# Optimization experiments

Hardware: AMD Instinct MI355X
Metric: run time of the kernel (lower is better)

The kernel has to match this reference:

```python
import jax, jax.numpy as jnp
import numpy as np

EPS = 1e-5

def mean_variance_norm(x):
    # x: [b,c,h,w]; torch .var(dim=2) on flattened spatial is UNBIASED (n-1)
    b, c, h, w = x.shape
    n = h * w
    mean = jnp.mean(x, axis=(2, 3), keepdims=True)
    var = jnp.sum((x - mean) ** 2, axis=(2, 3), keepdims=True) / (n - 1) + EPS
    return (x - mean) / jnp.sqrt(var)

def conv1x1(x, W, b):
    # 1x1 conv == channel-mixing matmul. W: [out_c, in_c], b: [out_c]
    return jnp.einsum('oc,bchw->bohw', W, x) + b[None, :, None, None]

def setup_inputs() -> dict:
    key = jax.random.key(0)
    ks = jax.random.split(key, 10)
    C = 512
    shp = (4, C, 64, 64)
    std = 1.0 / np.sqrt(C)
    return {
        'content': jax.random.normal(ks[0], shp, jnp.float32),
        'style': jax.random.normal(ks[1], shp, jnp.float32),
        'Wf': jax.random.normal(ks[2], (C, C), jnp.float32) * std,
        'bf': jax.random.normal(ks[3], (C,), jnp.float32) * 0.01,
        'Wg': jax.random.normal(ks[4], (C, C), jnp.float32) * std,
        'bg': jax.random.normal(ks[5], (C,), jnp.float32) * 0.01,
        'Wh': jax.random.normal(ks[6], (C, C), jnp.float32) * std,
        'bh': jax.random.normal(ks[7], (C,), jnp.float32) * 0.01,
        'Wo': jax.random.normal(ks[8], (C, C), jnp.float32) * std,
        'bo': jax.random.normal(ks[9], (C,), jnp.float32) * 0.01,
    }

def reference(content, style, Wf, bf, Wg, bg, Wh, bh, Wo, bo):
    b, c, h, w = content.shape
    hw = h * w
    F = conv1x1(mean_variance_norm(content), Wf, bf).reshape(b, c, hw)  # queries
    G = conv1x1(mean_variance_norm(style), Wg, bg).reshape(b, c, hw)    # keys
    H = conv1x1(style, Wh, bh).reshape(b, c, hw)                        # values
    # S[b,n,m] = sum_c F[b,c,n] * G[b,c,m]  (unscaled attention scores)
    S = jnp.einsum('bcn,bcm->bnm', F, G)
    S = jax.nn.softmax(S, axis=-1)
    # O[b,c,n] = sum_m H[b,c,m] * S[b,n,m]
    O = jnp.einsum('bcm,bnm->bcn', H, S).reshape(b, c, h, w)
    O = conv1x1(O, Wo, bo)
    return O + content
```

## Files before the change

### kernel.cpp

```cpp
#include <hip/hip_runtime.h>

#define C 512
#define HW 4096
#define EPSV 1e-5f

typedef _Float16 fp16x8 __attribute__((ext_vector_type(8)));
typedef _Float16 fp16x4 __attribute__((ext_vector_type(4)));
typedef float f32x4 __attribute__((ext_vector_type(4)));

#define OFF_MC    (0)
#define OFF_RC    (8192)
#define OFF_MS    (16384)
#define OFF_RS    (24576)
#define OFF_BETAF (32768)
#define OFF_V     (40960)
#define OFF_BZ    (49152)
#define OFF_T     (65536)
#define OFF_SP    (131072)
#define OFF_A     (OFF_SP + 2097152)
#define OFF_WZ    (OFF_A + 1048576)
#define OFF_XCT   (OFF_WZ + 1048576)
#define OFF_XST   (OFF_XCT + 16777216)
#define OFF_KT    (OFF_XST + 16777216)
#define OFF_HM    (OFF_KT + 16777216)
#define OFF_ML    (OFF_HM + 16777216)
#define OFF_S     (OFF_ML + 8388608)

#define FT_IDX(n, c) ((((size_t)((n) >> 4) * 16 + ((c) >> 5)) * 512) + \
                      ((((c) >> 3) & 3) * 128) + (((n) & 15) * 8) + ((c) & 7))

#define SFT_IDX(n, m) ((((size_t)((n) >> 4) * 128 + ((m) >> 5)) * 512) + \
                       ((((m) >> 3) & 3) * 128) + (((n) & 15) * 8) + ((m) & 7))


__global__ void transpose_stats_kernel(const float* __restrict__ xc, const float* __restrict__ xs,
                                       char* __restrict__ ws)
{
    int bx = blockIdx.x;
    int tensor = bx >> 11, b = (bx >> 9) & 3, c0 = ((bx >> 6) & 7) * 64, n0 = (bx & 63) * 64;
    const float* src = tensor ? xs : xc;
    _Float16* dst = (_Float16*)(ws + (tensor ? OFF_XST : OFF_XCT));
    float2* part = (float2*)(ws + OFF_SP);

    __shared__ _Float16 tile[64][72];
    __shared__ float sred[4][64], ssred[4][64];

    int tid = threadIdx.x, cR = tid & 63, ng = tid >> 6;
    const float* p = src + ((size_t)(b * C + c0 + cR)) * HW + n0 + ng * 16;
    float s = 0.f, ss = 0.f;
    #pragma unroll
    for (int k = 0; k < 4; k++) {
        float4 v = *(const float4*)(p + k * 4);
        s += v.x + v.y + v.z + v.w;
        ss += v.x * v.x + v.y * v.y + v.z * v.z + v.w * v.w;
        int n = ng * 16 + k * 4;
        tile[n][cR] = (_Float16)v.x; tile[n + 1][cR] = (_Float16)v.y;
        tile[n + 2][cR] = (_Float16)v.z; tile[n + 3][cR] = (_Float16)v.w;
    }
    sred[ng][cR] = s; ssred[ng][cR] = ss;
    __syncthreads();
    if (tid < 64) {
        float S = sred[0][tid] + sred[1][tid] + sred[2][tid] + sred[3][tid];
        float SS = ssred[0][tid] + ssred[1][tid] + ssred[2][tid] + ssred[3][tid];
        part[((size_t)((tensor * 4 + b) * 512 + c0 + tid)) * 64 + (n0 >> 6)] = make_float2(S, SS);
    }
    _Float16* dstB = dst + (size_t)b * HW * C;
    #pragma unroll
    for (int i = 0; i < 2; i++) {
        int g = tid + i * 256, row = g >> 3, c8 = (g & 7) * 8;
        int n = n0 + row, c = c0 + c8;
        *(fp16x8*)&dstB[FT_IDX(n, c)] = *(const fp16x8*)&tile[row][c8];
    }
}

__global__ void finalize_stats_kernel(char* __restrict__ ws)
{
    int ch = blockIdx.x * 256 + threadIdx.x;
    const float2* part = (const float2*)(ws + OFF_SP) + (size_t)ch * 64;
    float S = 0.f, SS = 0.f;
    for (int k = 0; k < 64; k++) { float2 v = part[k]; S += v.x; SS += v.y; }
    int tensor = ch >> 11, rem = ch & 2047;
    float m = S / (float)HW;
    float var = (SS - S * m) / (float)(HW - 1) + EPSV;
    ((float*)(ws + (tensor ? OFF_MS : OFF_MC)))[rem] = m;
    ((float*)(ws + (tensor ? OFF_RS : OFF_RC)))[rem] = rsqrtf(var);
}

__global__ void precompute_kernel(const float* __restrict__ Wf, const float* __restrict__ Wg,
                                  const float* __restrict__ Wo, const float* __restrict__ Wh,
                                  const float* __restrict__ bf, const float* __restrict__ bh,
                                  char* __restrict__ ws)
{
    float* A = (float*)(ws + OFF_A);
    float* Wz = (float*)(ws + OFF_WZ);
    float* betaf = (float*)(ws + OFF_BETAF);
    float* bz = (float*)(ws + OFF_BZ);
    const float* mc = (const float*)(ws + OFF_MC);
    const float* rc = (const float*)(ws + OFF_RC);
    int bx = blockIdx.x, t = threadIdx.x;
    if (bx < 512) {
        bool isA = bx < 256;
        int r0 = (isA ? bx : bx - 256) * 2;
        float a00 = 0.f, a01 = 0.f, a10 = 0.f, a11 = 0.f;
        for (int k = 0; k < C; k++) {
            float r0v, r1v, c0v, c1v;
            if (isA) {
                r0v = Wf[k * C + r0]; r1v = Wf[k * C + r0 + 1];
                c0v = Wg[k * C + t];  c1v = Wg[k * C + t + 256];
            } else {
                r0v = Wo[r0 * C + k]; r1v = Wo[(r0 + 1) * C + k];
                c0v = Wh[k * C + t];  c1v = Wh[k * C + t + 256];
            }
            a00 += r0v * c0v; a01 += r0v * c1v;
            a10 += r1v * c0v; a11 += r1v * c1v;
        }
        float* D = isA ? A : Wz;
        D[r0 * C + t] = a00;       D[r0 * C + t + 256] = a01;
        D[(r0 + 1) * C + t] = a10; D[(r0 + 1) * C + t + 256] = a11;
    } else if (bx < 520) {
        int g = (bx - 512) * 256 + t, b = g >> 9, co = g & 511;
        float acc = 0.f;
        for (int i = 0; i < C; i++) acc += Wf[co * C + i] * mc[b * C + i] * rc[b * C + i];
        betaf[g] = bf[co] - acc;
    } else {
        int co = (bx - 520) * 256 + t;
        float acc = 0.f;
        for (int i = 0; i < C; i++) acc += Wo[co * C + i] * bh[i];
        bz[co] = acc;
    }
}

__global__ void precompute_v_kernel(const float* __restrict__ Wg, char* __restrict__ ws)
{
    const float* betaf = (const float*)(ws + OFF_BETAF);
    const float* rs = (const float*)(ws + OFF_RS);
    float* v = (float*)(ws + OFF_V);
    int g = blockIdx.x * 32 + (threadIdx.x >> 3);
    int b = g >> 9, j = g & 511, cq = threadIdx.x & 7;
    float acc = 0.f;
    for (int co = cq * 64; co < cq * 64 + 64; co++) acc += betaf[b * C + co] * Wg[co * C + j];
    acc += __shfl_xor(acc, 1);
    acc += __shfl_xor(acc, 2);
    acc += __shfl_xor(acc, 4);
    if (cq == 0) v[g] = rs[b * C + j] * acc;
}

__global__ void __launch_bounds__(256) prep_gemm_kernel(char* __restrict__ ws)
{
    const float* A = (const float*)(ws + OFF_A);
    const float* Wz = (const float*)(ws + OFF_WZ);
    const float* rc = (const float*)(ws + OFF_RC);
    const float* rs = (const float*)(ws + OFF_RS);
    const float* bz = (const float*)(ws + OFF_BZ);
    const _Float16* __restrict__ xsT = (const _Float16*)(ws + OFF_XST);
    _Float16* __restrict__ Kt = (_Float16*)(ws + OFF_KT);
    _Float16* __restrict__ Hp = (_Float16*)(ws + OFF_HM);

    int bx = blockIdx.x;
    int b = bx & 3, rest = bx >> 2;
    int r128 = rest >> 5, mb = rest & 31;
    int r0 = r128 * 128, m0 = mb * 128;
    int w = threadIdx.x >> 6, lane = threadIdx.x & 63, q = lane >> 4, l16 = lane & 15;
    int wr = (w & 1) * 64, wm = (w >> 1) * 64;
    bool isK = (r0 < 512);
    const float* Asrc = isK ? A : Wz;
    int rbase = (isK ? r0 : r0 - 512) + wr;

    f32x4 zz = {0.f, 0.f, 0.f, 0.f};
    f32x4 acc[4][4];
    #pragma unroll
    for (int rt = 0; rt < 4; rt++)
        #pragma unroll
        for (int mt = 0; mt < 4; mt++) acc[rt][mt] = zz;

    float rcv[4];
    #pragma unroll
    for (int rt = 0; rt < 4; rt++)
        rcv[rt] = isK ? rc[b * C + rbase + rt * 16 + l16] : 1.f;

    const _Float16* xb = xsT + (size_t)b * HW * C
                             + (size_t)((m0 + wm) >> 4) * 8192 + q * 128 + l16 * 8;

    for (int ks = 0; ks < 16; ks++) {
        int j0 = ks * 32 + q * 8;
        float rsv[8];
        if (isK) {
            float4 u0 = *(const float4*)&rs[b * C + j0];
            float4 u1 = *(const float4*)&rs[b * C + j0 + 4];
            rsv[0] = u0.x; rsv[1] = u0.y; rsv[2] = u0.z; rsv[3] = u0.w;
            rsv[4] = u1.x; rsv[5] = u1.y; rsv[6] = u1.z; rsv[7] = u1.w;
        } else {
            #pragma unroll
            for (int jj = 0; jj < 8; jj++) rsv[jj] = 1.f;
        }
        fp16x8 afr[4];
        #pragma unroll
        for (int rt = 0; rt < 4; rt++) {
            int row = rbase + rt * 16 + l16;
            float4 a0 = *(const float4*)&Asrc[row * C + j0];
            float4 a1 = *(const float4*)&Asrc[row * C + j0 + 4];
            float av8[8];
            av8[0] = a0.x; av8[1] = a0.y; av8[2] = a0.z; av8[3] = a0.w;
            av8[4] = a1.x; av8[5] = a1.y; av8[6] = a1.z; av8[7] = a1.w;
            float sc = rcv[rt];
            #pragma unroll
            for (int jj = 0; jj < 8; jj++)
                afr[rt][jj] = (_Float16)(isK ? av8[jj] * sc * rsv[jj] : av8[jj]);
        }
        fp16x8 bfr[4];
        #pragma unroll
        for (int mt = 0; mt < 4; mt++)
            bfr[mt] = *(const fp16x8*)(xb + (size_t)(mt * 16 + ks) * 512);
        #pragma unroll
        for (int rt = 0; rt < 4; rt++)
            #pragma unroll
            for (int mt = 0; mt < 4; mt++)
                acc[rt][mt] = __builtin_amdgcn_mfma_f32_16x16x32_f16(afr[rt], bfr[mt], acc[rt][mt], 0, 0, 0);
    }

    if (isK) {
        _Float16* KtB = Kt + (size_t)b * HW * C;
        #pragma unroll
        for (int rt = 0; rt < 4; rt++)
            #pragma unroll
            for (int mt = 0; mt < 4; mt++) {
                int m = m0 + wm + mt * 16 + l16;
                int cb = r0 + wr + rt * 16 + q * 4;
                fp16x4 h;
                h[0] = (_Float16)acc[rt][mt][0]; h[1] = (_Float16)acc[rt][mt][1];
                h[2] = (_Float16)acc[rt][mt][2]; h[3] = (_Float16)acc[rt][mt][3];
                *(fp16x4*)&KtB[FT_IDX(m, cb)] = h;
            }
    } else {
        _Float16* HpB = Hp + (size_t)b * 2097152;
        #pragma unroll
        for (int rt = 0; rt < 4; rt++) {
            float bzv[4];
            #pragma unroll
            for (int reg = 0; reg < 4; reg++) bzv[reg] = bz[rbase + rt * 16 + q * 4 + reg];
            #pragma unroll
            for (int mt = 0; mt < 4; mt++) {
                int m = m0 + wm + mt * 16 + l16;
                int mbase = (m >> 3) * 128 + (m & 7);
                #pragma unroll
                for (int reg = 0; reg < 4; reg++) {
                    int co = rbase + rt * 16 + q * 4 + reg;
                    HpB[(size_t)(co >> 4) * 65536 + mbase + (co & 15) * 8] =
                        (_Float16)(acc[rt][mt][reg] + bzv[reg]);
                }
            }
        }
    }
}

__global__ void t_kernel(char* __restrict__ ws)
{
    const float* v = (const float*)(ws + OFF_V);
    const _Float16* __restrict__ xsT = (const _Float16*)(ws + OFF_XST);
    float* tG = (float*)(ws + OFF_T);
    int bx = blockIdx.x;
    int b = bx >> 7, m0 = (bx & 127) * 32;
    int m = m0 + (threadIdx.x >> 3), cq = threadIdx.x & 7;
    const _Float16* p = xsT + (size_t)b * HW * C + (size_t)(m >> 4) * 8192 + (m & 15) * 8;
    const float* vp = v + b * C + cq * 64;
    float acc = 0.f;
    #pragma unroll
    for (int k = 0; k < 8; k++) {
        fp16x8 xv = *(const fp16x8*)(p + (cq * 2 + (k >> 2)) * 512 + (k & 3) * 128);
        float4 v0 = *(const float4*)(vp + k * 8);
        float4 v1 = *(const float4*)(vp + k * 8 + 4);
        acc += (float)xv[0] * v0.x + (float)xv[1] * v0.y + (float)xv[2] * v0.z + (float)xv[3] * v0.w
             + (float)xv[4] * v1.x + (float)xv[5] * v1.y + (float)xv[6] * v1.z + (float)xv[7] * v1.w;
    }
    acc += __shfl_xor(acc, 1);
    acc += __shfl_xor(acc, 2);
    acc += __shfl_xor(acc, 4);
    if (cq == 0) tG[b * HW + m] = acc;
}

__global__ void __launch_bounds__(256, 4) qk_kernel(char* __restrict__ ws)
{
    const _Float16* __restrict__ xcT = (const _Float16*)(ws + OFF_XCT);
    const _Float16* __restrict__ Kt = (const _Float16*)(ws + OFF_KT);
    const float* __restrict__ tG = (const float*)(ws + OFF_T);
    float2* __restrict__ ML = (float2*)(ws + OFF_ML);
    _Float16* __restrict__ Sg = (_Float16*)(ws + OFF_S);

    int bx = blockIdx.x;
    int b = (bx >> 1) & 3, mhi = bx & 1;
    int rest = bx >> 3, mlo = rest & 15, ntile = rest >> 4;
    int m0 = (mhi * 16 + mlo) * 128, n0 = ntile * 128;
    int tid = threadIdx.x, w = tid >> 6, lane = tid & 63, q = lane >> 4, l16 = lane & 15;
    int wn = (w & 1) * 64, wm = (w >> 1) * 64;

    const _Float16* ab = xcT + (size_t)b * HW * C
                             + (size_t)((n0 + wn) >> 4) * 8192 + q * 128 + l16 * 8;
    const _Float16* bb = Kt + (size_t)b * HW * C
                            + (size_t)((m0 + wm) >> 4) * 8192 + q * 128 + l16 * 8;

    f32x4 zz = {0.f, 0.f, 0.f, 0.f};
    f32x4 acc[4][4];
    #pragma unroll
    for (int nt = 0; nt < 4; nt++)
        #pragma unroll
        for (int mt = 0; mt < 4; mt++) acc[nt][mt] = zz;

    #pragma unroll 4
    for (int ks = 0; ks < 16; ks++) {
        fp16x8 afr[4], bfr[4];
        #pragma unroll
        for (int nt = 0; nt < 4; nt++)
            afr[nt] = *(const fp16x8*)(ab + (size_t)(nt * 16 + ks) * 512);
        #pragma unroll
        for (int mt = 0; mt < 4; mt++)
            bfr[mt] = *(const fp16x8*)(bb + (size_t)(mt * 16 + ks) * 512);
        #pragma unroll
        for (int nt = 0; nt < 4; nt++)
            #pragma unroll
            for (int mt = 0; mt < 4; mt++)
                acc[nt][mt] = __builtin_amdgcn_mfma_f32_16x16x32_f16(afr[nt], bfr[mt], acc[nt][mt], 0, 0, 0);
    }

    float tv[4];
    #pragma unroll
    for (int mt = 0; mt < 4; mt++) tv[mt] = tG[b * HW + m0 + wm + mt * 16 + l16];
    #pragma unroll
    for (int nt = 0; nt < 4; nt++)
        #pragma unroll
        for (int mt = 0; mt < 4; mt++)
            #pragma unroll
            for (int reg = 0; reg < 4; reg++) acc[nt][mt][reg] += tv[mt];

    float rm[4][4], sum[4][4];
    #pragma unroll
    for (int nt = 0; nt < 4; nt++)
        #pragma unroll
        for (int reg = 0; reg < 4; reg++)
            rm[nt][reg] = fmaxf(fmaxf(acc[nt][0][reg], acc[nt][1][reg]),
                                fmaxf(acc[nt][2][reg], acc[nt][3][reg]));
    #pragma unroll
    for (int s = 1; s < 16; s <<= 1)
        #pragma unroll
        for (int nt = 0; nt < 4; nt++)
            #pragma unroll
            for (int reg = 0; reg < 4; reg++)
                rm[nt][reg] = fmaxf(rm[nt][reg], __shfl_xor(rm[nt][reg], s));
    #pragma unroll
    for (int nt = 0; nt < 4; nt++)
        #pragma unroll
        for (int reg = 0; reg < 4; reg++) sum[nt][reg] = 0.f;
    #pragma unroll
    for (int nt = 0; nt < 4; nt++)
        #pragma unroll
        for (int mt = 0; mt < 4; mt++)
            #pragma unroll
            for (int reg = 0; reg < 4; reg++) {
                float pv = __expf(acc[nt][mt][reg] - rm[nt][reg]);
                acc[nt][mt][reg] = pv;
                sum[nt][reg] += pv;
            }
    #pragma unroll
    for (int s = 1; s < 16; s <<= 1)
        #pragma unroll
        for (int nt = 0; nt < 4; nt++)
            #pragma unroll
            for (int reg = 0; reg < 4; reg++)
                sum[nt][reg] += __shfl_xor(sum[nt][reg], s);

    int tl = (m0 + wm) >> 6;
    if (l16 == 0) {
        #pragma unroll
        for (int nt = 0; nt < 4; nt++)
            #pragma unroll
            for (int reg = 0; reg < 4; reg++)
                ML[((size_t)(b * HW + n0 + wn + nt * 16 + q * 4 + reg)) * 64 + tl] =
                    make_float2(rm[nt][reg], sum[nt][reg]);
    }

    __shared__ _Float16 Pl[4][64][72];
    #pragma unroll
    for (int nt = 0; nt < 4; nt++)
        #pragma unroll
        for (int mt = 0; mt < 4; mt++)
            #pragma unroll
            for (int reg = 0; reg < 4; reg++)
                Pl[w][nt * 16 + q * 4 + reg][mt * 16 + l16] = (_Float16)acc[nt][mt][reg];
    __syncthreads();
    _Float16* SgB = Sg + (size_t)b * 16777216;
    #pragma unroll
    for (int i = 0; i < 8; i++) {
        int row = i * 8 + (lane >> 3), c8 = (lane & 7) * 8;
        int n = n0 + wn + row, m = m0 + wm + c8;
        *(fp16x8*)&SgB[SFT_IDX(n, m)] = *(const fp16x8*)&Pl[w][row][c8];
    }
}

__global__ void __launch_bounds__(256) scale_kernel(char* __restrict__ ws)
{
    const float* __restrict__ mlf0 = (const float*)(ws + OFF_ML);
    float* __restrict__ Scl = (float*)(ws + OFF_XCT);
    __shared__ float mlv[64][129];
    __shared__ float Ms[64], Li[64];

    int g0 = blockIdx.x * 64;
    int tid = threadIdx.x;
    const float* mlf = mlf0 + (size_t)g0 * 128;

    #pragma unroll
    for (int i = 0; i < 8; i++) {
        int f4 = i * 256 + tid;
        int row = f4 >> 5, c4 = (f4 & 31) * 4;
        float4 v = *(const float4*)(mlf + row * 128 + c4);
        mlv[row][c4] = v.x; mlv[row][c4 + 1] = v.y;
        mlv[row][c4 + 2] = v.z; mlv[row][c4 + 3] = v.w;
    }
    __syncthreads();
    if (tid < 64) {
        float M = -1e30f;
        #pragma unroll
        for (int k = 0; k < 64; k++) M = fmaxf(M, mlv[tid][k * 2]);
        float L = 0.f;
        #pragma unroll
        for (int k = 0; k < 64; k++) L += mlv[tid][k * 2 + 1] * __expf(mlv[tid][k * 2] - M);
        Ms[tid] = M; Li[tid] = 1.f / L;
    }
    __syncthreads();
    int b = g0 >> 12, nbase = g0 & 4095;
    float* sp = Scl + (size_t)b * 262144 + nbase;
    int row = tid & 63, tsub = tid >> 6;
    #pragma unroll
    for (int pass = 0; pass < 16; pass++) {
        int tile = pass * 4 + tsub;
        sp[(size_t)tile * 4096 + row] = __expf(mlv[row][tile * 2] - Ms[row]) * Li[row];
    }
}

__global__ void __launch_bounds__(256, 4) pv_kernel(const float* __restrict__ xc,
                                                    const float* __restrict__ bo,
                                                    float* __restrict__ out,
                                                    char* __restrict__ ws)
{
    const _Float16* __restrict__ Sft = (const _Float16*)(ws + OFF_S);
    const _Float16* __restrict__ Hp = (const _Float16*)(ws + OFF_HM);
    const float* __restrict__ Scl = (const float*)(ws + OFF_XCT);

    int bx = blockIdx.x;
    int b = bx & 3, cog = (bx >> 2) & 7, ntb = bx >> 5;
    int co0 = cog * 64;
    int tid = threadIdx.x, w = tid >> 6, lane = tid & 63, q = lane >> 4, l16 = lane & 15;
    int n0w = ntb * 128 + w * 32;

    __shared__ _Float16 Hl[2][4096];

    int ln64 = lane;
    const _Float16* hsrc = Hp + (size_t)b * 2097152
                              + (size_t)((co0 >> 4) + w) * 65536 + ln64 * 8;
    const _Float16* sb = Sft + (size_t)b * 16777216
                             + (size_t)(ntb * 8 + w * 2) * 65536 + q * 128 + l16 * 8;
    const float* sc = Scl + (size_t)b * 262144 + n0w + q * 4;

    {
        fp16x8 s0 = *(const fp16x8*)(hsrc);
        fp16x8 s1 = *(const fp16x8*)(hsrc + 512);
        *(fp16x8*)&Hl[0][w * 1024 + ln64 * 8] = s0;
        *(fp16x8*)&Hl[0][w * 1024 + 512 + ln64 * 8] = s1;
    }
    __syncthreads();

    f32x4 zz = {0.f, 0.f, 0.f, 0.f};
    f32x4 acc[2][4];
    #pragma unroll
    for (int nt = 0; nt < 2; nt++)
        #pragma unroll
        for (int ct = 0; ct < 4; ct++) acc[nt][ct] = zz;

    for (int chunk = 0; chunk < 64; chunk++) {
        int buf = chunk & 1;
        fp16x8 s0n, s1n;
        if (chunk < 63) {
            s0n = *(const fp16x8*)(hsrc + (chunk + 1) * 1024);
            s1n = *(const fp16x8*)(hsrc + (chunk + 1) * 1024 + 512);
        }

        f32x4 tmp[2][4];
        #pragma unroll
        for (int km = 0; km < 2; km++) {
            fp16x8 afr[2], bfr[4];
            #pragma unroll
            for (int nt = 0; nt < 2; nt++)
                afr[nt] = *(const fp16x8*)(sb + (size_t)nt * 65536 + (chunk * 2 + km) * 512);
            #pragma unroll
            for (int ct = 0; ct < 4; ct++)
                bfr[ct] = *(const fp16x8*)&Hl[buf][ct * 1024 + (km * 4 + q) * 128 + l16 * 8];
            #pragma unroll
            for (int nt = 0; nt < 2; nt++)
                #pragma unroll
                for (int ct = 0; ct < 4; ct++)
                    tmp[nt][ct] = __builtin_amdgcn_mfma_f32_16x16x32_f16(
                        afr[nt], bfr[ct], km == 0 ? zz : tmp[nt][ct], 0, 0, 0);
        }
        float4 sv0 = *(const float4*)(sc + chunk * 4096);
        float4 sv1 = *(const float4*)(sc + chunk * 4096 + 16);
        float sva[2][4] = {{sv0.x, sv0.y, sv0.z, sv0.w}, {sv1.x, sv1.y, sv1.z, sv1.w}};
        #pragma unroll
        for (int nt = 0; nt < 2; nt++)
            #pragma unroll
            for (int ct = 0; ct < 4; ct++)
                #pragma unroll
                for (int reg = 0; reg < 4; reg++)
                    acc[nt][ct][reg] += tmp[nt][ct][reg] * sva[nt][reg];

        if (chunk < 63) {
            *(fp16x8*)&Hl[buf ^ 1][w * 1024 + ln64 * 8] = s0n;
            *(fp16x8*)&Hl[buf ^ 1][w * 1024 + 512 + ln64 * 8] = s1n;
        }
        __syncthreads();
    }

    #pragma unroll
    for (int nt = 0; nt < 2; nt++)
        #pragma unroll
        for (int ct = 0; ct < 4; ct++) {
            int co = co0 + ct * 16 + l16;
            size_t base = ((size_t)(b * C + co)) * HW + n0w + nt * 16 + q * 4;
            float4 cv = *(const float4*)&xc[base];
            float bov = bo[co];
            float4 o;
            o.x = acc[nt][ct][0] + bov + cv.x;
            o.y = acc[nt][ct][1] + bov + cv.y;
            o.z = acc[nt][ct][2] + bov + cv.z;
            o.w = acc[nt][ct][3] + bov + cv.w;
            *(float4*)&out[base] = o;
        }
}

extern "C" void kernel_launch(void* const* d_in, const int* in_sizes, int n_in,
                              void* d_out, int out_size, void* d_ws, size_t ws_size,
                              hipStream_t stream)
{
    const float* content = (const float*)d_in[0];
    const float* style   = (const float*)d_in[1];
    const float* Wf = (const float*)d_in[2];
    const float* bf = (const float*)d_in[3];
    const float* Wg = (const float*)d_in[4];
    const float* Wh = (const float*)d_in[6];
    const float* bh = (const float*)d_in[7];
    const float* Wo = (const float*)d_in[8];
    const float* bo = (const float*)d_in[9];
    float* out = (float*)d_out;
    char* ws = (char*)d_ws;

    transpose_stats_kernel<<<4096, 256, 0, stream>>>(content, style, ws);
    finalize_stats_kernel<<<16, 256, 0, stream>>>(ws);
    precompute_kernel<<<522, 256, 0, stream>>>(Wf, Wg, Wo, Wh, bf, bh, ws);
    precompute_v_kernel<<<64, 256, 0, stream>>>(Wg, ws);
    prep_gemm_kernel<<<1024, 256, 0, stream>>>(ws);
    t_kernel<<<512, 256, 0, stream>>>(ws);
    qk_kernel<<<4096, 256, 0, stream>>>(ws);
    scale_kernel<<<256, 256, 0, stream>>>(ws);
    pv_kernel<<<1024, 256, 0, stream>>>(content, bo, out, ws);
}
```

Before: 506.8 us.

## Prescale and pack projection weights to fp16 tiles, coalesce stats and t kernels

```diff
diff --git a/kernel.cpp b/kernel.cpp
--- a/kernel.cpp
+++ b/kernel.cpp
@@ -43,26 +43,28 @@
     float2* part = (float2*)(ws + OFF_SP);
 
     __shared__ _Float16 tile[64][72];
-    __shared__ float sred[4][64], ssred[4][64];
-
-    int tid = threadIdx.x, cR = tid & 63, ng = tid >> 6;
-    const float* p = src + ((size_t)(b * C + c0 + cR)) * HW + n0 + ng * 16;
-    float s = 0.f, ss = 0.f;
+    __shared__ float sredL[64], ssredL[64];
+
+    int tid = threadIdx.x, w = tid >> 6, lane = tid & 63, cq = lane >> 4, l16 = lane & 15;
     #pragma unroll
     for (int k = 0; k < 4; k++) {
-        float4 v = *(const float4*)(p + k * 4);
-        s += v.x + v.y + v.z + v.w;
-        ss += v.x * v.x + v.y * v.y + v.z * v.z + v.w * v.w;
-        int n = ng * 16 + k * 4;
-        tile[n][cR] = (_Float16)v.x; tile[n + 1][cR] = (_Float16)v.y;
-        tile[n + 2][cR] = (_Float16)v.z; tile[n + 3][cR] = (_Float16)v.w;
-    }
-    sred[ng][cR] = s; ssred[ng][cR] = ss;
+        int cr = w * 16 + k * 4 + cq;
+        int nf = l16 * 4;
+        float4 v = *(const float4*)(src + ((size_t)(b * C + c0 + cr)) * HW + n0 + nf);
+        float s = v.x + v.y + v.z + v.w;
+        float ss = v.x * v.x + v.y * v.y + v.z * v.z + v.w * v.w;
+        s += __shfl_xor(s, 1); ss += __shfl_xor(ss, 1);
+        s += __shfl_xor(s, 2); ss += __shfl_xor(ss, 2);
+        s += __shfl_xor(s, 4); ss += __shfl_xor(ss, 4);
+        s += __shfl_xor(s, 8); ss += __shfl_xor(ss, 8);
+        if (l16 == 0) { sredL[cr] = s; ssredL[cr] = ss; }
+        tile[nf][cr] = (_Float16)v.x; tile[nf + 1][cr] = (_Float16)v.y;
+        tile[nf + 2][cr] = (_Float16)v.z; tile[nf + 3][cr] = (_Float16)v.w;
+    }
     __syncthreads();
     if (tid < 64) {
-        float S = sred[0][tid] + sred[1][tid] + sred[2][tid] + sred[3][tid];
-        float SS = ssred[0][tid] + ssred[1][tid] + ssred[2][tid] + ssred[3][tid];
-        part[((size_t)((tensor * 4 + b) * 512 + c0 + tid)) * 64 + (n0 >> 6)] = make_float2(S, SS);
+        part[((size_t)((tensor * 4 + b) * 512 + c0 + tid)) * 64 + (n0 >> 6)] =
+            make_float2(sredL[tid], ssredL[tid]);
     }
     _Float16* dstB = dst + (size_t)b * HW * C;
     #pragma unroll
@@ -92,7 +94,7 @@
                                   char* __restrict__ ws)
 {
     float* A = (float*)(ws + OFF_A);
-    float* Wz = (float*)(ws + OFF_WZ);
+    _Float16* Wz16 = (_Float16*)(ws + OFF_WZ);
     float* betaf = (float*)(ws + OFF_BETAF);
     float* bz = (float*)(ws + OFF_BZ);
     const float* mc = (const float*)(ws + OFF_MC);
@@ -114,9 +116,15 @@
             a00 += r0v * c0v; a01 += r0v * c1v;
             a10 += r1v * c0v; a11 += r1v * c1v;
         }
-        float* D = isA ? A : Wz;
-        D[r0 * C + t] = a00;       D[r0 * C + t + 256] = a01;
-        D[(r0 + 1) * C + t] = a10; D[(r0 + 1) * C + t + 256] = a11;
+        if (isA) {
+            A[r0 * C + t] = a00;       A[r0 * C + t + 256] = a01;
+            A[(r0 + 1) * C + t] = a10; A[(r0 + 1) * C + t + 256] = a11;
+        } else {
+            Wz16[FT_IDX(r0, t)] = (_Float16)a00;
+            Wz16[FT_IDX(r0, t + 256)] = (_Float16)a01;
+            Wz16[FT_IDX(r0 + 1, t)] = (_Float16)a10;
+            Wz16[FT_IDX(r0 + 1, t + 256)] = (_Float16)a11;
+        }
     } else if (bx < 520) {
         int g = (bx - 512) * 256 + t, b = g >> 9, co = g & 511;
         float acc = 0.f;
@@ -128,6 +136,33 @@
         for (int i = 0; i < C; i++) acc += Wo[co * C + i] * bh[i];
         bz[co] = acc;
     }
+}
+
+__global__ void scaleA_kernel(char* __restrict__ ws)
+{
+    const float* __restrict__ A = (const float*)(ws + OFF_A);
+    const float* __restrict__ rc = (const float*)(ws + OFF_RC);
+    const float* __restrict__ rs = (const float*)(ws + OFF_RS);
+    _Float16* __restrict__ As = (_Float16*)(ws + OFF_SP);
+
+    int gid = blockIdx.x * 256 + threadIdx.x;
+    int b = gid >> 15, rem = gid & 32767;
+    int sub = rem >> 6, low6 = rem & 63;
+    int r16 = sub >> 4, cb4 = sub & 15;
+    int q = low6 >> 4, l16 = low6 & 15;
+    int r = r16 * 16 + l16, j0 = (cb4 * 4 + q) * 8;
+
+    float4 a0 = *(const float4*)&A[r * C + j0];
+    float4 a1 = *(const float4*)&A[r * C + j0 + 4];
+    float4 s0 = *(const float4*)&rs[b * C + j0];
+    float4 s1 = *(const float4*)&rs[b * C + j0 + 4];
+    float rcv = rc[b * C + r];
+    fp16x8 o;
+    o[0] = (_Float16)(a0.x * rcv * s0.x); o[1] = (_Float16)(a0.y * rcv * s0.y);
+    o[2] = (_Float16)(a0.z * rcv * s0.z); o[3] = (_Float16)(a0.w * rcv * s0.w);
+    o[4] = (_Float16)(a1.x * rcv * s1.x); o[5] = (_Float16)(a1.y * rcv * s1.y);
+    o[6] = (_Float16)(a1.z * rcv * s1.z); o[7] = (_Float16)(a1.w * rcv * s1.w);
+    *(fp16x8*)&As[(size_t)b * 262144 + (size_t)sub * 512 + low6 * 8] = o;
 }
 
 __global__ void precompute_v_kernel(const float* __restrict__ Wg, char* __restrict__ ws)
@@ -147,11 +182,9 @@
 
 __global__ void __launch_bounds__(256) prep_gemm_kernel(char* __restrict__ ws)
 {
-    const float* A = (const float*)(ws + OFF_A);
-    const float* Wz = (const float*)(ws + OFF_WZ);
-    const float* rc = (const float*)(ws + OFF_RC);
-    const float* rs = (const float*)(ws + OFF_RS);
-    const float* bz = (const float*)(ws + OFF_BZ);
+    const _Float16* __restrict__ As = (const _Float16*)(ws + OFF_SP);
+    const _Float16* __restrict__ Wz16 = (const _Float16*)(ws + OFF_WZ);
+    const float* __restrict__ bz = (const float*)(ws + OFF_BZ);
     const _Float16* __restrict__ xsT = (const _Float16*)(ws + OFF_XST);
     _Float16* __restrict__ Kt = (_Float16*)(ws + OFF_KT);
     _Float16* __restrict__ Hp = (_Float16*)(ws + OFF_HM);
@@ -163,7 +196,6 @@
     int w = threadIdx.x >> 6, lane = threadIdx.x & 63, q = lane >> 4, l16 = lane & 15;
     int wr = (w & 1) * 64, wm = (w >> 1) * 64;
     bool isK = (r0 < 512);
-    const float* Asrc = isK ? A : Wz;
     int rbase = (isK ? r0 : r0 - 512) + wr;
 
     f32x4 zz = {0.f, 0.f, 0.f, 0.f};
@@ -173,41 +205,16 @@
         #pragma unroll
         for (int mt = 0; mt < 4; mt++) acc[rt][mt] = zz;
 
-    float rcv[4];
-    #pragma unroll
-    for (int rt = 0; rt < 4; rt++)
-        rcv[rt] = isK ? rc[b * C + rbase + rt * 16 + l16] : 1.f;
-
+    const _Float16* ap = (isK ? As + (size_t)b * 262144 : Wz16)
+                         + (size_t)(rbase >> 4) * 8192 + q * 128 + l16 * 8;
     const _Float16* xb = xsT + (size_t)b * HW * C
                              + (size_t)((m0 + wm) >> 4) * 8192 + q * 128 + l16 * 8;
 
     for (int ks = 0; ks < 16; ks++) {
-        int j0 = ks * 32 + q * 8;
-        float rsv[8];
-        if (isK) {
-            float4 u0 = *(const float4*)&rs[b * C + j0];
-            float4 u1 = *(const float4*)&rs[b * C + j0 + 4];
-            rsv[0] = u0.x; rsv[1] = u0.y; rsv[2] = u0.z; rsv[3] = u0.w;
-            rsv[4] = u1.x; rsv[5] = u1.y; rsv[6] = u1.z; rsv[7] = u1.w;
-        } else {
-            #pragma unroll
-            for (int jj = 0; jj < 8; jj++) rsv[jj] = 1.f;
-        }
-        fp16x8 afr[4];
-        #pragma unroll
-        for (int rt = 0; rt < 4; rt++) {
-            int row = rbase + rt * 16 + l16;
-            float4 a0 = *(const float4*)&Asrc[row * C + j0];
-            float4 a1 = *(const float4*)&Asrc[row * C + j0 + 4];
-            float av8[8];
-            av8[0] = a0.x; av8[1] = a0.y; av8[2] = a0.z; av8[3] = a0.w;
-            av8[4] = a1.x; av8[5] = a1.y; av8[6] = a1.z; av8[7] = a1.w;
-            float sc = rcv[rt];
-            #pragma unroll
-            for (int jj = 0; jj < 8; jj++)
-                afr[rt][jj] = (_Float16)(isK ? av8[jj] * sc * rsv[jj] : av8[jj]);
-        }
-        fp16x8 bfr[4];
+        fp16x8 afr[4], bfr[4];
+        #pragma unroll
+        for (int rt = 0; rt < 4; rt++)
+            afr[rt] = *(const fp16x8*)(ap + (size_t)rt * 8192 + ks * 512);
         #pragma unroll
         for (int mt = 0; mt < 4; mt++)
             bfr[mt] = *(const fp16x8*)(xb + (size_t)(mt * 16 + ks) * 512);
@@ -259,23 +266,23 @@
     const _Float16* __restrict__ xsT = (const _Float16*)(ws + OFF_XST);
     float* tG = (float*)(ws + OFF_T);
     int bx = blockIdx.x;
-    int b = bx >> 7, m0 = (bx & 127) * 32;
-    int m = m0 + (threadIdx.x >> 3), cq = threadIdx.x & 7;
-    const _Float16* p = xsT + (size_t)b * HW * C + (size_t)(m >> 4) * 8192 + (m & 15) * 8;
-    const float* vp = v + b * C + cq * 64;
+    int b = bx >> 6, mb = bx & 63;
+    int tid = threadIdx.x, w = tid >> 6, lane = tid & 63, q = lane >> 4, l16 = lane & 15;
+    int M16 = mb * 4 + w;
+    const _Float16* p = xsT + (size_t)b * HW * C + (size_t)M16 * 8192 + q * 128 + l16 * 8;
+    const float* vp = v + b * C + q * 8;
     float acc = 0.f;
     #pragma unroll
-    for (int k = 0; k < 8; k++) {
-        fp16x8 xv = *(const fp16x8*)(p + (cq * 2 + (k >> 2)) * 512 + (k & 3) * 128);
-        float4 v0 = *(const float4*)(vp + k * 8);
-        float4 v1 = *(const float4*)(vp + k * 8 + 4);
+    for (int st = 0; st < 16; st++) {
+        fp16x8 xv = *(const fp16x8*)(p + st * 512);
+        float4 v0 = *(const float4*)(vp + st * 32);
+        float4 v1 = *(const float4*)(vp + st * 32 + 4);
         acc += (float)xv[0] * v0.x + (float)xv[1] * v0.y + (float)xv[2] * v0.z + (float)xv[3] * v0.w
              + (float)xv[4] * v1.x + (float)xv[5] * v1.y + (float)xv[6] * v1.z + (float)xv[7] * v1.w;
     }
-    acc += __shfl_xor(acc, 1);
-    acc += __shfl_xor(acc, 2);
-    acc += __shfl_xor(acc, 4);
-    if (cq == 0) tG[b * HW + m] = acc;
+    acc += __shfl_xor(acc, 16);
+    acc += __shfl_xor(acc, 32);
+    if (q == 0) tG[b * HW + M16 * 16 + l16] = acc;
 }
 
 __global__ void __launch_bounds__(256, 4) qk_kernel(char* __restrict__ ws)
@@ -553,9 +560,10 @@
     transpose_stats_kernel<<<4096, 256, 0, stream>>>(content, style, ws);
     finalize_stats_kernel<<<16, 256, 0, stream>>>(ws);
     precompute_kernel<<<522, 256, 0, stream>>>(Wf, Wg, Wo, Wh, bf, bh, ws);
+    scaleA_kernel<<<512, 256, 0, stream>>>(ws);
     precompute_v_kernel<<<64, 256, 0, stream>>>(Wg, ws);
     prep_gemm_kernel<<<1024, 256, 0, stream>>>(ws);
-    t_kernel<<<512, 256, 0, stream>>>(ws);
+    t_kernel<<<256, 256, 0, stream>>>(ws);
     qk_kernel<<<4096, 256, 0, stream>>>(ws);
     scale_kernel<<<256, 256, 0, stream>>>(ws);
     pv_kernel<<<1024, 256, 0, stream>>>(content, bo, out, ws);
```

Result: faster. 465.7 us (-8.1%).
